# Performance work log

Measured on AMD Instinct MI355X. Metric: run time of the kernel, lower is better.

## Reference

```python
import jax, jax.numpy as jnp
import numpy as np

B, T, D = 8, 1024, 1024
H = 16
DH = D // H  # 64


def setup_inputs() -> dict:
    key = jax.random.key(0)
    k1, k2, k3 = jax.random.split(key, 3)
    x = jax.random.normal(k1, (B, T, D), dtype=jnp.float32)
    W_qkv = jax.random.normal(k2, (3 * D, D), dtype=jnp.float32) * (D ** -0.5)
    W_proj = jax.random.normal(k3, (D, D), dtype=jnp.float32) * (D ** -0.5)
    return {"x": x, "W_qkv": W_qkv, "W_proj": W_proj}


def reference(x, W_qkv, W_proj):
    b, t, _ = x.shape
    # qkv: [B,T,3*D] -> [B,T,3,H,DH]
    qkv = (x @ W_qkv.T).reshape(b, t, 3, H, DH)
    q, k, v = qkv[:, :, 0], qkv[:, :, 1], qkv[:, :, 2]  # [B,T,H,DH]
    scale = DH ** -0.5
    # scores: [B,H,Tq,Tk]
    scores = jnp.einsum("bqhd,bkhd->bhqk", q, k) * scale
    # NOTE: softmax over dim=-2 (the QUERY axis), as in the original module
    attn = jax.nn.softmax(scores, axis=-2)
    out = jnp.einsum("bhqk,bkhd->bqhd", attn, v).reshape(b, t, D)
    return out @ W_proj.T
```

## Files before the change

### kernel.cpp

```cpp
#include <hip/hip_runtime.h>


typedef __bf16 bf16_t;
typedef __bf16 bf16x8 __attribute__((ext_vector_type(8)));
typedef __bf16 bf16x4 __attribute__((ext_vector_type(4)));
typedef float f32x4 __attribute__((ext_vector_type(4)));
typedef unsigned short u16x8 __attribute__((ext_vector_type(8)));

#define DEV __device__ __forceinline__
#define C2 0.18033688f

DEV void gld_lds16(const bf16_t* g, bf16_t* l) {
  __builtin_amdgcn_global_load_lds(
      (const __attribute__((address_space(1))) unsigned int*)g,
      (__attribute__((address_space(3))) unsigned int*)l, 16, 0, 0);
}

DEV float exp2c(float x) { return __builtin_amdgcn_exp2f(fminf(x, 30.f)); }
DEV float sanit(float v) { return (v == v) ? fminf(fmaxf(v, -1e4f), 1e4f) : 0.f; }

DEV int sw64(int r, int kc) { return r * 64 + (((kc ^ (r + (r >> 3))) & 7) << 3); }

DEV f32x4 mfma16(bf16x8 a, bf16x8 b, f32x4 c) {
  return __builtin_amdgcn_mfma_f32_16x16x32_bf16(a, b, c, 0, 0, 0);
}

__global__ void detect_dtype(const unsigned short* x, int* flag) {
  __shared__ int smax;
  if (threadIdx.x == 0) smax = 0;
  __syncthreads();
  int m = 0;
  for (int i = threadIdx.x; i < 16384; i += 256) {
    int e = (x[i] >> 7) & 0xFF;
    m = m > e ? m : e;
  }
  atomicMax(&smax, m);
  __syncthreads();
  if (threadIdx.x == 0) *flag = (smax >= 160) ? 1 : 0;
}

__global__ void convert_in(const void* __restrict__ x, const void* __restrict__ wq,
                           const void* __restrict__ wp, bf16_t* __restrict__ xb,
                           bf16_t* __restrict__ wqb, bf16_t* __restrict__ wpb,
                           const int* __restrict__ flag) {
  int i = blockIdx.x * 256 + threadIdx.x;
  const void* src;
  bf16_t* dst;
  int off;
  bool isQ = false;
  if (i < 1048576) { src = x; dst = xb; off = i; }
  else if (i < 1441792) {
    src = wq; dst = wqb; off = i - 1048576;
    isQ = off < 131072;
  } else { src = wp; dst = wpb; off = i - 1441792; }
  if (*flag) {
    const float s = isQ ? C2 : 1.0f;
    const float4* sp = (const float4*)src;
    float4 a = sp[off * 2], b = sp[off * 2 + 1];
    bf16x8 o;
    o[0] = (bf16_t)(a.x * s); o[1] = (bf16_t)(a.y * s);
    o[2] = (bf16_t)(a.z * s); o[3] = (bf16_t)(a.w * s);
    o[4] = (bf16_t)(b.x * s); o[5] = (bf16_t)(b.y * s);
    o[6] = (bf16_t)(b.z * s); o[7] = (bf16_t)(b.w * s);
    *(bf16x8*)(dst + (size_t)off * 8) = o;
  } else {
    u16x8 v = ((const u16x8*)src)[off];
    if (isQ) {
      bf16x8 bsrc = __builtin_bit_cast(bf16x8, v);
      bf16x8 o;
#pragma unroll
      for (int t = 0; t < 8; ++t) o[t] = (bf16_t)((float)bsrc[t] * C2);
      *(bf16x8*)(dst + (size_t)off * 8) = o;
    } else {
      ((u16x8*)dst)[off] = v;
    }
  }
}

__global__ __launch_bounds__(256, 2)
void gemm_bt(const bf16_t* __restrict__ A, int lda, const bf16_t* __restrict__ B,
             bf16_t* __restrict__ Cb, float* __restrict__ Cf, int ldc,
             int K, const int* __restrict__ f32flag) {
  __shared__ bf16_t sA0[128 * 64];
  __shared__ bf16_t sB0[128 * 64];
  __shared__ bf16_t sA1[128 * 64];
  __shared__ bf16_t sB1[128 * 64];
  const int tid = threadIdx.x;
  const int wave = tid >> 6, lane = tid & 63;
  const int l = lane & 15, quad = lane >> 4;
  const int nwg = gridDim.x * gridDim.y;
  const int bid = blockIdx.y * gridDim.x + blockIdx.x;
  const int sb = (bid & 7) * (nwg >> 3) + (bid >> 3);
  const int row0 = (sb / gridDim.x) * 128, col0 = (sb % gridDim.x) * 128;
  const int wm = (wave >> 1) * 64, wn = (wave & 1) * 64;
  f32x4 acc[4][4];
#pragma unroll
  for (int i = 0; i < 4; ++i)
#pragma unroll
    for (int j = 0; j < 4; ++j) acc[i][j] = f32x4{0.f, 0.f, 0.f, 0.f};

#define STAGE_G(sa, sb_, kk)                                                  \
  {                                                                           \
    _Pragma("unroll") for (int t = 0; t < 4; ++t) {                           \
      int n = t * 256 + tid;                                                  \
      int r = n >> 3;                                                         \
      int kc = ((n & 7) ^ (r + (r >> 3))) & 7;                                \
      gld_lds16(A + (size_t)(row0 + r) * lda + (kk) + kc * 8, (sa) + n * 8);  \
      gld_lds16(B + (size_t)(col0 + r) * K + (kk) + kc * 8, (sb_) + n * 8);   \
    }                                                                         \
  }

#define COMPUTE_G(sa, sb_)                                                    \
  {                                                                           \
    _Pragma("unroll") for (int ks = 0; ks < 2; ++ks) {                        \
      bf16x8 af[4], bfr[4];                                                   \
      _Pragma("unroll") for (int i = 0; i < 4; ++i) af[i] =                   \
          *(const bf16x8*)&(sa)[sw64(wm + i * 16 + l, ks * 4 + quad)];        \
      _Pragma("unroll") for (int j = 0; j < 4; ++j) bfr[j] =                  \
          *(const bf16x8*)&(sb_)[sw64(wn + j * 16 + l, ks * 4 + quad)];       \
      _Pragma("unroll") for (int i = 0; i < 4; ++i)                           \
          _Pragma("unroll") for (int j = 0; j < 4; ++j) acc[i][j] =           \
              mfma16(af[i], bfr[j], acc[i][j]);                               \
    }                                                                         \
  }

  STAGE_G(sA0, sB0, 0);
  for (int k0 = 0; k0 < K; k0 += 128) {
    __syncthreads();
    if (k0 + 64 < K) STAGE_G(sA1, sB1, k0 + 64);
    COMPUTE_G(sA0, sB0);
    __syncthreads();
    if (k0 + 128 < K) STAGE_G(sA0, sB0, k0 + 128);
    COMPUTE_G(sA1, sB1);
  }
#undef STAGE_G
#undef COMPUTE_G

  const bool of32 = (f32flag != nullptr) && (*f32flag != 0);
#pragma unroll
  for (int i = 0; i < 4; ++i) {
    int rr = row0 + wm + i * 16 + quad * 4;
#pragma unroll
    for (int j = 0; j < 4; ++j) {
      int cc = col0 + wn + j * 16 + l;
#pragma unroll
      for (int t = 0; t < 4; ++t) {
        float v = sanit(acc[i][j][t]);
        size_t idx = (size_t)(rr + t) * ldc + cc;
        if (of32) Cf[idx] = v; else Cb[idx] = (bf16_t)v;
      }
    }
  }
}

__global__ __launch_bounds__(256, 4)
void attn_stats(const bf16_t* __restrict__ qkv, bf16_t* __restrict__ Vts) {
  __shared__ bf16_t sK[128 * 64];
  __shared__ bf16_t sV[128 * 64];
  __shared__ float sL[128];
  const int bh = blockIdx.x, kt = blockIdx.y;
  const int b = bh >> 4, h = bh & 15;
  const int tid = threadIdx.x, wave = tid >> 6, lane = tid & 63;
  const int l = lane & 15, quad = lane >> 4;
  const size_t rowK = (size_t)b * 1024 + kt * 128;

#pragma unroll
  for (int t = 0; t < 4; ++t) {
    int base = wave * 256 + t * 64;
    int n = base + lane;
    int r = n >> 3;
    int kc = ((n & 7) ^ (r + (r >> 3))) & 7;
    gld_lds16(qkv + (rowK + r) * 3072 + 2048 + h * 64 + kc * 8, sV + base * 8);
    gld_lds16(qkv + (rowK + r) * 3072 + 1024 + h * 64 + kc * 8, sK + base * 8);
  }
  if (tid < 128) sL[tid] = 0.f;
  __syncthreads();

  float accj[8];
#pragma unroll
  for (int j = 0; j < 8; ++j) accj[j] = 0.f;

  for (int qt = 0; qt < 8; ++qt) {
    bf16x8 aq[2][2];
#pragma unroll
    for (int i = 0; i < 2; ++i)
#pragma unroll
      for (int ks = 0; ks < 2; ++ks)
        aq[i][ks] = *(const bf16x8*)&qkv[((size_t)b * 1024 + qt * 128 + wave * 32 +
                                          i * 16 + l) * 3072 + h * 64 +
                                         (ks * 4 + quad) * 8];
#pragma unroll
    for (int j = 0; j < 8; ++j) {
      f32x4 s0 = {0.f, 0.f, 0.f, 0.f}, s1 = {0.f, 0.f, 0.f, 0.f};
#pragma unroll
      for (int ks = 0; ks < 2; ++ks) {
        bf16x8 bk = *(const bf16x8*)&sK[sw64(j * 16 + l, ks * 4 + quad)];
        s0 = mfma16(aq[0][ks], bk, s0);
        s1 = mfma16(aq[1][ks], bk, s1);
      }
#pragma unroll
      for (int t = 0; t < 4; ++t)
        accj[j] += exp2c(s0[t]) + exp2c(s1[t]);
    }
  }
#pragma unroll
  for (int j = 0; j < 8; ++j) {
    float v = accj[j];
    v += __shfl_xor(v, 16);
    v += __shfl_xor(v, 32);
    if (lane < 16) atomicAdd(&sL[j * 16 + l], v);
  }
  __syncthreads();
  if (tid < 128) sL[tid] = 1.0f / fmaxf(sL[tid], 1e-20f);
  __syncthreads();

#pragma unroll
  for (int t = 0; t < 4; ++t) {
    int u = t * 256 + tid;
    int d = u >> 4, k0 = (u & 15) * 8;
    bf16x8 pk;
#pragma unroll
    for (int i = 0; i < 8; ++i) {
      int kl = (k0 & ~31) | ((i >> 2) << 4) | (((k0 >> 3) & 3) << 2) | (i & 3);
      float v = (float)sV[sw64(kl, d >> 3) + (d & 7)];
      pk[i] = (bf16_t)(v * sL[kl]);
    }
    *(bf16x8*)&Vts[((size_t)bh * 64 + d) * 1024 + kt * 128 + k0] = pk;
  }
}

__global__ __launch_bounds__(512, 4)
void attn_out_k(const bf16_t* __restrict__ qkv, const bf16_t* __restrict__ Vts,
                bf16_t* __restrict__ attn) {
  __shared__ bf16_t sK[2][128 * 64];
  __shared__ bf16_t sV[2][64 * 128];
  const int bh = blockIdx.x, qt = blockIdx.y;
  const int b = bh >> 4, h = bh & 15;
  const int tid = threadIdx.x, wave = tid >> 6, lane = tid & 63;
  const int l = lane & 15, quad = lane >> 4;
  const bf16_t* qbase = qkv + (size_t)b * 3145728 + h * 64;
  const bf16_t* vbase = Vts + (size_t)bh * 65536;

  bf16x8 bq[2][2];
#pragma unroll
  for (int i = 0; i < 2; ++i)
#pragma unroll
    for (int ks = 0; ks < 2; ++ks)
      bq[i][ks] = *(const bf16x8*)&qbase[(size_t)(qt * 256 + wave * 32 + i * 16 + l) *
                                             3072 + ks * 32 + quad * 8];
  f32x4 o[2][4];
#pragma unroll
  for (int i = 0; i < 2; ++i)
#pragma unroll
    for (int jd = 0; jd < 4; ++jd) o[i][jd] = f32x4{0.f, 0.f, 0.f, 0.f};

#pragma unroll
  for (int t = 0; t < 2; ++t) {
    int n = t * 512 + tid;
    int r = n >> 3;
    int kc = ((n & 7) ^ (r + (r >> 3))) & 7;
    gld_lds16(qkv + ((size_t)b * 1024 + r) * 3072 + 1024 + h * 64 + kc * 8,
              sK[0] + n * 8);
    int d = n >> 4, s = n & 15;
    int c = s ^ (d & 7);
    gld_lds16(vbase + (size_t)d * 1024 + c * 8, sV[0] + n * 8);
  }

  for (int kt = 0; kt < 8; ++kt) {
    const int buf = kt & 1;
    __syncthreads();
    if (kt < 7) {
#pragma unroll
      for (int t = 0; t < 2; ++t) {
        int n = t * 512 + tid;
        int r = n >> 3;
        int kc = ((n & 7) ^ (r + (r >> 3))) & 7;
        gld_lds16(qkv + ((size_t)b * 1024 + (kt + 1) * 128 + r) * 3072 + 1024 +
                      h * 64 + kc * 8,
                  sK[buf ^ 1] + n * 8);
        int d = n >> 4, s = n & 15;
        int c = s ^ (d & 7);
        gld_lds16(vbase + (size_t)d * 1024 + (kt + 1) * 128 + c * 8,
                  sV[buf ^ 1] + n * 8);
      }
    }
    const bf16_t* sKb = sK[buf];
    const bf16_t* sVb = sV[buf];

#pragma unroll
    for (int ch = 0; ch < 4; ++ch) {
      bf16x8 ak[2][2];
#pragma unroll
      for (int kk = 0; kk < 2; ++kk)
#pragma unroll
        for (int ks = 0; ks < 2; ++ks)
          ak[kk][ks] = *(const bf16x8*)&sKb[sw64(ch * 32 + kk * 16 + l,
                                                 ks * 4 + quad)];
      bf16x8 va[4];
#pragma unroll
      for (int jd = 0; jd < 4; ++jd)
        va[jd] = *(const bf16x8*)&sVb[(jd * 16 + l) * 128 +
                                      (((ch * 4 + quad) ^ (l & 7)) << 3)];
#pragma unroll
      for (int i = 0; i < 2; ++i) {
        __builtin_amdgcn_s_setprio(1);
        f32x4 st0 = {0.f, 0.f, 0.f, 0.f}, st1 = {0.f, 0.f, 0.f, 0.f};
        st0 = mfma16(ak[0][0], bq[i][0], st0);
        st0 = mfma16(ak[0][1], bq[i][1], st0);
        st1 = mfma16(ak[1][0], bq[i][0], st1);
        st1 = mfma16(ak[1][1], bq[i][1], st1);
        bf16x8 pc;
#pragma unroll
        for (int t = 0; t < 4; ++t) {
          pc[t] = (bf16_t)exp2c(st0[t]);
          pc[4 + t] = (bf16_t)exp2c(st1[t]);
        }
#pragma unroll
        for (int jd = 0; jd < 4; ++jd)
          o[i][jd] = mfma16(va[jd], pc, o[i][jd]);
        __builtin_amdgcn_s_setprio(0);
      }
    }
  }
#pragma unroll
  for (int i = 0; i < 2; ++i) {
    size_t row = (size_t)b * 1024 + qt * 256 + wave * 32 + i * 16 + l;
#pragma unroll
    for (int jd = 0; jd < 4; ++jd) {
      bf16x4 pk;
#pragma unroll
      for (int t = 0; t < 4; ++t) pk[t] = (bf16_t)sanit(o[i][jd][t]);
      *(bf16x4*)&attn[row * 3072 + h * 64 + jd * 16 + quad * 4] = pk;
    }
  }
}

extern "C" void kernel_launch(void* const* d_in, const int* in_sizes, int n_in,
                              void* d_out, int out_size, void* d_ws, size_t ws_size,
                              hipStream_t stream) {
  (void)in_sizes; (void)n_in; (void)out_size; (void)ws_size;
  char* w = (char*)d_ws;
  bf16_t* qkv = (bf16_t*)w;
  bf16_t* xb = (bf16_t*)(w + 50331648);
  bf16_t* Vts = xb;
  bf16_t* Wqkvb = (bf16_t*)(w + 67108864);
  bf16_t* Wprojb = (bf16_t*)(w + 73400320);
  int* flag = (int*)(w + 75497472);
  bf16_t* attn = qkv + 2048;

  detect_dtype<<<1, 256, 0, stream>>>((const unsigned short*)d_in[0], flag);
  convert_in<<<6144, 256, 0, stream>>>(d_in[0], d_in[1], d_in[2],
                                       xb, Wqkvb, Wprojb, flag);

  gemm_bt<<<dim3(24, 64), 256, 0, stream>>>(xb, 1024, Wqkvb, qkv, nullptr, 3072,
                                            1024, nullptr);
  attn_stats<<<dim3(128, 8), 256, 0, stream>>>(qkv, Vts);
  attn_out_k<<<dim3(128, 4), 512, 0, stream>>>(qkv, Vts, attn);
  gemm_bt<<<dim3(8, 64), 256, 0, stream>>>(attn, 3072, Wprojb, (bf16_t*)d_out,
                                           (float*)d_out, 1024, 1024, flag);
}
```

Before: 271.9 us.

## Restructure GEMM K-loop pipeline with explicit waitcnt and register-staged fragments

The GEMM main loop now keeps two global-to-LDS stages in flight. It loads all LDS fragments for a 64-wide K tile into registers with inline-asm ds_read_b128, then issues the next global prefetch into the same buffer before running the MFMAs. Fine-grained s_waitcnt vmcnt/lgkmcnt and sched_barriers replace the generic __syncthreads, so global loads overlap compute more deeply. This raises register pressure because fragments for both k-substeps are held at once. It also depends on the exact vmcnt count (8 loads per stage) staying correct.

```diff
diff --git a/kernel.cpp b/kernel.cpp
--- a/kernel.cpp
+++ b/kernel.cpp
@@ -23,6 +23,14 @@
 
 DEV f32x4 mfma16(bf16x8 a, bf16x8 b, f32x4 c) {
   return __builtin_amdgcn_mfma_f32_16x16x32_bf16(a, b, c, 0, 0, 0);
+}
+
+DEV unsigned ldsa(const bf16_t* p) { return (unsigned)(size_t)p; }
+
+DEV bf16x8 dsr128(unsigned addr) {
+  bf16x8 r;
+  asm volatile("ds_read_b128 %0, %1" : "=v"(r) : "v"(addr));
+  return r;
 }
 
 __global__ void detect_dtype(const unsigned short* x, int* flag) {
@@ -110,31 +118,62 @@
     }                                                                         \
   }
 
-#define COMPUTE_G(sa, sb_)                                                    \
+#define LOADFRAGS(sa, sb_, af_, bf_)                                          \
   {                                                                           \
     _Pragma("unroll") for (int ks = 0; ks < 2; ++ks) {                        \
-      bf16x8 af[4], bfr[4];                                                   \
-      _Pragma("unroll") for (int i = 0; i < 4; ++i) af[i] =                   \
-          *(const bf16x8*)&(sa)[sw64(wm + i * 16 + l, ks * 4 + quad)];        \
-      _Pragma("unroll") for (int j = 0; j < 4; ++j) bfr[j] =                  \
-          *(const bf16x8*)&(sb_)[sw64(wn + j * 16 + l, ks * 4 + quad)];       \
       _Pragma("unroll") for (int i = 0; i < 4; ++i)                           \
-          _Pragma("unroll") for (int j = 0; j < 4; ++j) acc[i][j] =           \
-              mfma16(af[i], bfr[j], acc[i][j]);                               \
+          af_[ks][i] =                                                        \
+              dsr128(ldsa(&(sa)[sw64(wm + i * 16 + l, ks * 4 + quad)]));      \
+      _Pragma("unroll") for (int j = 0; j < 4; ++j)                           \
+          bf_[ks][j] =                                                        \
+              dsr128(ldsa(&(sb_)[sw64(wn + j * 16 + l, ks * 4 + quad)]));     \
     }                                                                         \
   }
 
+#define MFMA_ALL(af_, bf_)                                                    \
+  {                                                                           \
+    _Pragma("unroll") for (int ks = 0; ks < 2; ++ks)                          \
+        _Pragma("unroll") for (int i = 0; i < 4; ++i)                         \
+            _Pragma("unroll") for (int j = 0; j < 4; ++j) acc[i][j] =         \
+                mfma16(af_[ks][i], bf_[ks][j], acc[i][j]);                    \
+  }
+
   STAGE_G(sA0, sB0, 0);
+  STAGE_G(sA1, sB1, 64);
+
   for (int k0 = 0; k0 < K; k0 += 128) {
-    __syncthreads();
-    if (k0 + 64 < K) STAGE_G(sA1, sB1, k0 + 64);
-    COMPUTE_G(sA0, sB0);
-    __syncthreads();
-    if (k0 + 128 < K) STAGE_G(sA0, sB0, k0 + 128);
-    COMPUTE_G(sA1, sB1);
+    asm volatile("s_waitcnt vmcnt(8)");
+    __builtin_amdgcn_sched_barrier(0);
+    __builtin_amdgcn_s_barrier();
+    {
+      bf16x8 af[2][4], bfr[2][4];
+      LOADFRAGS(sA0, sB0, af, bfr);
+      asm volatile("s_waitcnt lgkmcnt(0)");
+      __builtin_amdgcn_sched_barrier(0);
+      __builtin_amdgcn_s_barrier();
+      if (k0 + 128 < K) STAGE_G(sA0, sB0, k0 + 128);
+      MFMA_ALL(af, bfr);
+    }
+    if (k0 + 128 < K) {
+      asm volatile("s_waitcnt vmcnt(8)");
+    } else {
+      asm volatile("s_waitcnt vmcnt(0)");
+    }
+    __builtin_amdgcn_sched_barrier(0);
+    __builtin_amdgcn_s_barrier();
+    {
+      bf16x8 af[2][4], bfr[2][4];
+      LOADFRAGS(sA1, sB1, af, bfr);
+      asm volatile("s_waitcnt lgkmcnt(0)");
+      __builtin_amdgcn_sched_barrier(0);
+      __builtin_amdgcn_s_barrier();
+      if (k0 + 192 < K) STAGE_G(sA1, sB1, k0 + 192);
+      MFMA_ALL(af, bfr);
+    }
   }
 #undef STAGE_G
-#undef COMPUTE_G
+#undef LOADFRAGS
+#undef MFMA_ALL
 
   const bool of32 = (f32flag != nullptr) && (*f32flag != 0);
 #pragma unroll
```

After: 279.2 us. 1.03x slower.

## Replace QKV projection GEMM with 256x256-tile, 512-thread pipelined kernel

Applied to the files above, without the earlier changes.

Adds a dedicated QKV GEMM that uses 256x256 output tiles with eight waves. It stages 32-wide K slices into four swizzled LDS buffers through direct global-to-LDS loads, and orders loads and MFMA work using inline-asm ds_read, explicit vmcnt waits and priority hints. The larger tile is meant to raise operand reuse per byte loaded and hide global load latency behind MFMA work. The cost is many more accumulator registers, hand-tuned wait counts that must match the issue order, and a grid that only fits this shape (384 blocks).

```diff
diff --git a/kernel.cpp b/kernel.cpp
--- a/kernel.cpp
+++ b/kernel.cpp
@@ -20,9 +20,18 @@
 DEV float sanit(float v) { return (v == v) ? fminf(fmaxf(v, -1e4f), 1e4f) : 0.f; }
 
 DEV int sw64(int r, int kc) { return r * 64 + (((kc ^ (r + (r >> 3))) & 7) << 3); }
+DEV int sw32(int r, int kc) { return r * 32 + (((kc ^ r ^ (r >> 2)) & 3) << 3); }
 
 DEV f32x4 mfma16(bf16x8 a, bf16x8 b, f32x4 c) {
   return __builtin_amdgcn_mfma_f32_16x16x32_bf16(a, b, c, 0, 0, 0);
+}
+
+DEV unsigned ldsa(const bf16_t* p) { return (unsigned)(size_t)p; }
+
+DEV bf16x8 dsr128(unsigned addr) {
+  bf16x8 r;
+  asm volatile("ds_read_b128 %0, %1" : "=v"(r) : "v"(addr));
+  return r;
 }
 
 __global__ void detect_dtype(const unsigned short* x, int* flag) {
@@ -77,6 +86,109 @@
   }
 }
 
+__global__ __launch_bounds__(512, 2)
+void gemm256(const bf16_t* __restrict__ A, const bf16_t* __restrict__ Bm,
+             bf16_t* __restrict__ Cb) {
+  __shared__ bf16_t aL00[256 * 32];
+  __shared__ bf16_t aL01[256 * 32];
+  __shared__ bf16_t aL10[256 * 32];
+  __shared__ bf16_t aL11[256 * 32];
+  __shared__ bf16_t bL00[256 * 32];
+  __shared__ bf16_t bL01[256 * 32];
+  __shared__ bf16_t bL10[256 * 32];
+  __shared__ bf16_t bL11[256 * 32];
+  const int tid = threadIdx.x;
+  const int wave = tid >> 6, lane = tid & 63;
+  const int l = lane & 15, quad = lane >> 4;
+  const int wr = wave >> 2, wc = wave & 3;
+  const int bid = blockIdx.y * gridDim.x + blockIdx.x;
+  const int sb = (bid & 7) * 48 + (bid >> 3);
+  const int row0 = (sb / 12) * 256, col0 = (sb % 12) * 256;
+
+  f32x4 acc[8][4];
+#pragma unroll
+  for (int i = 0; i < 8; ++i)
+#pragma unroll
+    for (int j = 0; j < 4; ++j) acc[i][j] = f32x4{0.f, 0.f, 0.f, 0.f};
+
+#define STAGE1(XA, XB, koff, s)                                               \
+  {                                                                           \
+    int n = (s) * 512 + tid;                                                  \
+    int r = n >> 2;                                                           \
+    int kc = ((n & 3) ^ r ^ (r >> 2)) & 3;                                    \
+    gld_lds16(A + (size_t)(row0 + r) * 1024 + (koff) + kc * 8, (XA) + n * 8); \
+    gld_lds16(Bm + (size_t)(col0 + r) * 1024 + (koff) + kc * 8, (XB) + n * 8);\
+  }
+
+#define QPHASE(XA, XB, mh)                                                    \
+  {                                                                           \
+    bf16x8 af[4], bfv[4];                                                     \
+    _Pragma("unroll") for (int mi = 0; mi < 4; ++mi) af[mi] =                 \
+        dsr128(ldsa(&(XA)[sw32(wr * 128 + (mh) * 64 + mi * 16 + l, quad)]));  \
+    _Pragma("unroll") for (int ni = 0; ni < 4; ++ni) bfv[ni] =                \
+        dsr128(ldsa(&(XB)[sw32(wc * 64 + ni * 16 + l, quad)]));               \
+    asm volatile("s_waitcnt lgkmcnt(0)" ::: "memory");                        \
+    __builtin_amdgcn_sched_barrier(0);                                        \
+    __builtin_amdgcn_s_setprio(1);                                            \
+    _Pragma("unroll") for (int mi = 0; mi < 4; ++mi)                          \
+        _Pragma("unroll") for (int ni = 0; ni < 4; ++ni)                      \
+            acc[(mh) * 4 + mi][ni] =                                          \
+                mfma16(af[mi], bfv[ni], acc[(mh) * 4 + mi][ni]);              \
+    __builtin_amdgcn_s_setprio(0);                                            \
+  }
+
+#define TILE(A0, A1, B0, B1, NA1, NB1, t, S1ON, S2ON, VM0, VM2)               \
+  {                                                                           \
+    asm volatile("s_waitcnt " VM0 ::: "memory");                              \
+    __builtin_amdgcn_sched_barrier(0);                                        \
+    __builtin_amdgcn_s_barrier();                                             \
+    if (S1ON) STAGE1(NA1, NB1, (t) * 64 + 96, 0);                             \
+    QPHASE(A0, B0, 0);                                                        \
+    __builtin_amdgcn_s_barrier();                                             \
+    if (S1ON) STAGE1(NA1, NB1, (t) * 64 + 96, 1);                             \
+    QPHASE(A0, B0, 1);                                                        \
+    asm volatile("s_waitcnt " VM2 ::: "memory");                              \
+    __builtin_amdgcn_sched_barrier(0);                                        \
+    __builtin_amdgcn_s_barrier();                                             \
+    if (S2ON) STAGE1(A0, B0, (t) * 64 + 128, 0);                              \
+    QPHASE(A1, B1, 0);                                                        \
+    __builtin_amdgcn_s_barrier();                                             \
+    if (S2ON) STAGE1(A0, B0, (t) * 64 + 128, 1);                              \
+    QPHASE(A1, B1, 1);                                                        \
+  }
+
+  STAGE1(aL00, bL00, 0, 0);
+  STAGE1(aL00, bL00, 0, 1);
+  STAGE1(aL01, bL01, 32, 0);
+  STAGE1(aL01, bL01, 32, 1);
+  STAGE1(aL10, bL10, 64, 0);
+  STAGE1(aL10, bL10, 64, 1);
+
+  for (int it = 0; it < 7; ++it) {
+    const int t0 = 2 * it, t1 = 2 * it + 1;
+    TILE(aL00, aL01, bL00, bL01, aL11, bL11, t0, 1, 1, "vmcnt(8)", "vmcnt(8)");
+    TILE(aL10, aL11, bL10, bL11, aL01, bL01, t1, 1, 1, "vmcnt(8)", "vmcnt(8)");
+  }
+  TILE(aL00, aL01, bL00, bL01, aL11, bL11, 14, 1, 0, "vmcnt(8)", "vmcnt(8)");
+  TILE(aL10, aL11, bL10, bL11, aL01, bL01, 15, 0, 0, "vmcnt(4)", "vmcnt(0)");
+
+#undef TILE
+#undef QPHASE
+#undef STAGE1
+
+#pragma unroll
+  for (int mt = 0; mt < 8; ++mt) {
+    int rbase = row0 + wr * 128 + mt * 16 + quad * 4;
+#pragma unroll
+    for (int ni = 0; ni < 4; ++ni) {
+      int cc = col0 + wc * 64 + ni * 16 + l;
+#pragma unroll
+      for (int tt = 0; tt < 4; ++tt)
+        Cb[(size_t)(rbase + tt) * 3072 + cc] = (bf16_t)sanit(acc[mt][ni][tt]);
+    }
+  }
+}
+
 __global__ __launch_bounds__(256, 2)
 void gemm_bt(const bf16_t* __restrict__ A, int lda, const bf16_t* __restrict__ B,
              bf16_t* __restrict__ Cb, float* __restrict__ Cf, int ldc,
@@ -352,8 +464,7 @@
   convert_in<<<6144, 256, 0, stream>>>(d_in[0], d_in[1], d_in[2],
                                        xb, Wqkvb, Wprojb, flag);
 
-  gemm_bt<<<dim3(24, 64), 256, 0, stream>>>(xb, 1024, Wqkvb, qkv, nullptr, 3072,
-                                            1024, nullptr);
+  gemm256<<<dim3(12, 32), 512, 0, stream>>>(xb, Wqkvb, qkv);
   attn_stats<<<dim3(128, 8), 256, 0, stream>>>(qkv, Vts);
   attn_out_k<<<dim3(128, 4), 512, 0, stream>>>(qkv, Vts, attn);
   gemm_bt<<<dim3(8, 64), 256, 0, stream>>>(attn, 3072, Wprojb, (bf16_t*)d_out,
```

Result: slower. 284.3 us (+4.6%).
